# Optimization experiments

Hardware: AMD Instinct MI355X
Metric: run time of the kernel (lower is better)

## Reference

```python
import jax, jax.numpy as jnp
import numpy as np

B, S, H, NH = 2, 2048, 1024, 16
HD = H // NH  # 64


def setup_inputs() -> dict:
    key = jax.random.key(0)
    ks = jax.random.split(key, 9)
    w = lambda k: jax.random.normal(k, (H, H), dtype=jnp.float32) * 0.02  # torch Linear weight [out,in]
    b = lambda k: jax.random.normal(k, (H,), dtype=jnp.float32) * 0.02
    return {
        "hidden_states": jax.random.normal(ks[0], (B, S, H), dtype=jnp.float32),
        "Wq": w(ks[1]), "bq": b(ks[2]),
        "Wk": w(ks[3]), "bk": b(ks[4]),
        "Wv": w(ks[5]), "bv": b(ks[6]),
        "Wo": w(ks[7]), "bo": b(ks[8]),
    }


def reference(hidden_states, Wq, bq, Wk, bk, Wv, bv, Wo, bo):
    b, s, h = hidden_states.shape
    nh, hd = NH, h // NH

    def proj(W, bias):
        y = hidden_states @ W.T + bias  # torch Linear: x W^T + b
        return y.reshape(b, s, nh, hd).transpose(0, 2, 1, 3)  # [b, h, s, d]

    q = proj(Wq, bq)
    k = proj(Wk, bk)
    v = proj(Wv, bv)

    scale = jnp.sqrt(jnp.asarray(hd, dtype=q.dtype))
    scores = jnp.einsum("bhqd,bhkd->bhqk", q, k) / scale  # [b, h, s, s]
    pos = jnp.arange(s)
    causal = pos[:, None] < pos[None, :]  # True where masked (key after query)
    scores = jnp.where(causal[None, None], -jnp.inf, scores)
    attn = jax.nn.softmax(scores, axis=-1)
    out = jnp.einsum("bhqk,bhkd->bhqd", attn, v)
    out = out.transpose(0, 2, 1, 3).reshape(b, s, h)
    return out @ Wo.T + bo
```

## Files before the change

### kernel.cpp

```cpp
#include <hip/hip_runtime.h>
#include <stdint.h>

typedef __bf16 bf16;
typedef __attribute__((ext_vector_type(2))) __bf16 bf16x2;
typedef __attribute__((ext_vector_type(4))) __bf16 bf16x4;
typedef __attribute__((ext_vector_type(8))) __bf16 bf16x8;
typedef __attribute__((ext_vector_type(4))) float f32x4;
typedef __attribute__((ext_vector_type(4))) short s16x4;

#define B_  2
#define S_  2048
#define H_  1024
#define NH_ 16
#define HD_ 64

__device__ __forceinline__ void glds16(const bf16* g, bf16* l) {
  __builtin_amdgcn_global_load_lds(
      (const __attribute__((address_space(1))) uint32_t*)g,
      (__attribute__((address_space(3))) uint32_t*)l, 16, 0, 0);
}

__device__ __forceinline__ f32x4 pv_mfma(bf16x4 a, bf16x4 b, f32x4 c) {
#if __has_builtin(__builtin_amdgcn_mfma_f32_16x16x16bf16_1k)
  union U { bf16x4 h; s16x4 s; };
  U ua; ua.h = a;
  U ub; ub.h = b;
  return __builtin_amdgcn_mfma_f32_16x16x16bf16_1k(ua.s, ub.s, c, 0, 0, 0);
#else
  f32x4 d;
  asm volatile("v_mfma_f32_16x16x16_bf16 %0, %1, %2, %3\n\ts_nop 7\n\ts_nop 7"
               : "=v"(d) : "v"(a), "v"(b), "v"(c));
  return d;
#endif
}

__global__ __launch_bounds__(256) void cvt_f32_bf16(
    const float* __restrict__ s0, bf16* __restrict__ d0, int n0,
    const float* __restrict__ s1, bf16* __restrict__ d1,
    const float* __restrict__ s2, bf16* __restrict__ d2,
    const float* __restrict__ s3, bf16* __restrict__ d3,
    const float* __restrict__ s4, bf16* __restrict__ d4, int nw)
{
  const float* s; bf16* d; int n;
  switch (blockIdx.y) {
    case 0:  s = s0; d = d0; n = n0; break;
    case 1:  s = s1; d = d1; n = nw; break;
    case 2:  s = s2; d = d2; n = nw; break;
    case 3:  s = s3; d = d3; n = nw; break;
    default: s = s4; d = d4; n = nw; break;
  }
  const int i = (blockIdx.x * 256 + threadIdx.x) * 8;
  if (i >= n) return;
  float4 v0 = *(const float4*)(s + i);
  float4 v1 = *(const float4*)(s + i + 4);
  bf16x8 o;
  o[0] = (bf16)v0.x; o[1] = (bf16)v0.y; o[2] = (bf16)v0.z; o[3] = (bf16)v0.w;
  o[4] = (bf16)v1.x; o[5] = (bf16)v1.y; o[6] = (bf16)v1.z; o[7] = (bf16)v1.w;
  *(bf16x8*)(d + i) = o;
}

template <typename TY>
__global__ __launch_bounds__(256) void gemm_bt_bias(
    const bf16* __restrict__ X,
    const bf16* __restrict__ W0, const bf16* __restrict__ W1, const bf16* __restrict__ W2,
    const float* __restrict__ b0, const float* __restrict__ b1, const float* __restrict__ b2,
    TY* __restrict__ Y0, TY* __restrict__ Y1, TY* __restrict__ Y2,
    float ys0, float ys1, float ys2,
    int M, int N, int K)
{
  const bf16* W; const float* bias; TY* Y; float ysc;
  if (blockIdx.z == 0)      { W = W0; bias = b0; Y = Y0; ysc = ys0; }
  else if (blockIdx.z == 1) { W = W1; bias = b1; Y = Y1; ysc = ys1; }
  else                      { W = W2; bias = b2; Y = Y2; ysc = ys2; }

  __shared__ __align__(16) bf16 As[2][128 * 32];
  __shared__ __align__(16) bf16 Bs[2][128 * 32];

  const int tid  = threadIdx.x;
  const int lane = tid & 63;
  const int wave = tid >> 6;
  const int m0 = blockIdx.y * 128;
  const int n0 = blockIdx.x * 128;
  const int wm = (wave >> 1) * 64;
  const int wn = (wave & 1) * 64;

  const int r0 = tid >> 2,            c0 = (tid & 3) * 8;
  const int r1 = (256 + tid) >> 2,    c1 = ((256 + tid) & 3) * 8;
  const int cb0 = (wave * 64) * 8;
  const int cb1 = (256 + wave * 64) * 8;

  f32x4 acc[4][4] = {};

  glds16(X + (size_t)(m0 + r0) * K + c0, &As[0][cb0]);
  glds16(W + (size_t)(n0 + r0) * K + c0, &Bs[0][cb0]);
  glds16(X + (size_t)(m0 + r1) * K + c1, &As[0][cb1]);
  glds16(W + (size_t)(n0 + r1) * K + c1, &Bs[0][cb1]);

  int pb = 0;
  for (int k0 = 0; k0 < K; k0 += 32, pb ^= 1) {
    __syncthreads();

    if (k0 + 32 < K) {
      const int kn = k0 + 32;
      glds16(X + (size_t)(m0 + r0) * K + kn + c0, &As[pb ^ 1][cb0]);
      glds16(W + (size_t)(n0 + r0) * K + kn + c0, &Bs[pb ^ 1][cb0]);
      glds16(X + (size_t)(m0 + r1) * K + kn + c1, &As[pb ^ 1][cb1]);
      glds16(W + (size_t)(n0 + r1) * K + kn + c1, &Bs[pb ^ 1][cb1]);
    }

    bf16x8 a[4], b[4];
#pragma unroll
    for (int i = 0; i < 4; ++i)
      a[i] = *(const bf16x8*)&As[pb][(wm + i * 16 + (lane & 15)) * 32 + (lane >> 4) * 8];
#pragma unroll
    for (int i = 0; i < 4; ++i)
      b[i] = *(const bf16x8*)&Bs[pb][(wn + i * 16 + (lane & 15)) * 32 + (lane >> 4) * 8];
#pragma unroll
    for (int mi = 0; mi < 4; ++mi)
#pragma unroll
      for (int ni = 0; ni < 4; ++ni)
        acc[mi][ni] = __builtin_amdgcn_mfma_f32_16x16x32_bf16(a[mi], b[ni], acc[mi][ni], 0, 0, 0);
  }

#pragma unroll
  for (int mi = 0; mi < 4; ++mi) {
    const int row = m0 + wm + mi * 16 + (lane >> 4) * 4;
#pragma unroll
    for (int ni = 0; ni < 4; ++ni) {
      const int col = n0 + wn + ni * 16 + (lane & 15);
      const float bv = bias[col];
#pragma unroll
      for (int r = 0; r < 4; ++r)
        Y[(size_t)(row + r) * N + col] = (TY)((acc[mi][ni][r] + bv) * ysc);
    }
  }
}


__device__ __forceinline__ void attn_tile_step(
    const bf16* Ksb, const bf16* Vtb, const bf16x8 bq[2], int qrow, int k0,
    bool maskit, float& mr, float& lr, f32x4 oacc[4], int l15, int quad)
{
  f32x4 sacc[8] = {};
  __builtin_amdgcn_s_setprio(1);
#pragma unroll
  for (int ks = 0; ks < 2; ++ks) {
#pragma unroll
    for (int mb = 0; mb < 8; ++mb) {
      const int row = mb * 16 + l15;
      const int ch  = (ks * 4 + quad) ^ (l15 & 7);
      bf16x8 ak = *(const bf16x8*)&Ksb[row * 64 + ch * 8];
      sacc[mb] = __builtin_amdgcn_mfma_f32_16x16x32_bf16(ak, bq[ks], sacc[mb], 0, 0, 0);
    }
  }
  __builtin_amdgcn_s_setprio(0);

  if (maskit) {
#pragma unroll
    for (int mb = 0; mb < 8; ++mb) {
      const int kb = k0 + mb * 16 + quad * 4;
#pragma unroll
      for (int r = 0; r < 4; ++r)
        if (kb + r > qrow) sacc[mb][r] = -1e30f;
    }
  }

  float mx = -1e30f;
#pragma unroll
  for (int mb = 0; mb < 8; ++mb)
    mx = fmaxf(mx, fmaxf(fmaxf(sacc[mb][0], sacc[mb][1]),
                         fmaxf(sacc[mb][2], sacc[mb][3])));
  mx = fmaxf(mx, __shfl_xor(mx, 16, 64));
  mx = fmaxf(mx, __shfl_xor(mx, 32, 64));

  float sum = 0.0f;
  bf16x4 pwv[8];
#pragma unroll
  for (int mb = 0; mb < 8; ++mb) {
    bf16x4 pw;
#pragma unroll
    for (int r = 0; r < 4; ++r) {
      const float p = __builtin_amdgcn_exp2f(sacc[mb][r] - mr);
      sum += p;
      pw[r] = (bf16)p;
    }
    pwv[mb] = pw;
  }
  sum += __shfl_xor(sum, 16, 64);
  sum += __shfl_xor(sum, 32, 64);

  __builtin_amdgcn_s_setprio(1);
#pragma unroll
  for (int mb = 0; mb < 8; ++mb) {
#pragma unroll
    for (int db = 0; db < 4; ++db) {
      const int vch = ((mb * 4 + quad) ^ (l15 & 7)) * 4;
      bf16x4 av = *(const bf16x4*)&Vtb[(db * 16 + l15) * 128 + vch];
      oacc[db] = pv_mfma(av, pwv[mb], oacc[db]);
    }
  }
  __builtin_amdgcn_s_setprio(0);

  lr += sum;
  if (!__all(mx <= mr + 8.0f)) {
    const float mnew  = fmaxf(mr, mx);
    const float alpha = __builtin_amdgcn_exp2f(mr - mnew);
    lr *= alpha;
#pragma unroll
    for (int db = 0; db < 4; ++db)
#pragma unroll
      for (int r = 0; r < 4; ++r) oacc[db][r] *= alpha;
    mr = mnew;
  }
}

__global__ __launch_bounds__(256, 2) void attn_causal(
    const bf16* __restrict__ Q, const bf16* __restrict__ K,
    const bf16* __restrict__ V, bf16* __restrict__ O)
{
  const int lin  = blockIdx.x;
  const int slot = lin >> 3;
  const int bh   = (lin & 7) * 4 + (slot >> 4);
  const int pair = slot & 15;
  const int b    = bh >> 4;
  const int h    = bh & 15;

  const int tid  = threadIdx.x;
  const int lane = tid & 63;
  const int wave = tid >> 6;
  const int quad = lane >> 4;
  const int l15  = lane & 15;
  const size_t headoff = (size_t)b * S_ * H_ + (size_t)h * HD_;
  const bf16* Kp = K + headoff;
  const bf16* Vp = V + headoff;

  __shared__ __align__(16) bf16 Ks[2][128 * 64];
  __shared__ __align__(16) bf16 Vt[2][64 * 128];

  const int qlo = pair, qhi = 31 - pair;
  const int nl  = (qlo >> 1) + 1;
  const int nh  = (qhi >> 1) + 1;
  const int qrowL = qlo * 64 + wave * 16 + l15;
  const int qrowH = qhi * 64 + wave * 16 + l15;

  bf16x8 bqL[2], bqH[2];
  bqL[0] = *(const bf16x8*)(Q + headoff + (size_t)qrowL * H_ + quad * 8);
  bqL[1] = *(const bf16x8*)(Q + headoff + (size_t)qrowL * H_ + 32 + quad * 8);
  bqH[0] = *(const bf16x8*)(Q + headoff + (size_t)qrowH * H_ + quad * 8);
  bqH[1] = *(const bf16x8*)(Q + headoff + (size_t)qrowH * H_ + 32 + quad * 8);

  const int vr = lane * 2;
  const int vc = wave * 16;

#define STAGE_K(k0_, buf_)                                                  \
  {                                                                         \
    _Pragma("unroll")                                                       \
    for (int i = 0; i < 4; ++i) {                                           \
      const int n = i * 256 + tid;                                          \
      const int row = n >> 3;                                               \
      const int cg  = (n & 7) ^ (row & 7);                                  \
      glds16(Kp + (size_t)((k0_) + row) * H_ + cg * 8,                      \
             &Ks[buf_][(i * 256 + wave * 64) * 8]);                         \
    }                                                                       \
  }

#define LOAD_V(k0_)                                                         \
  {                                                                         \
    vreg[0] = *(const bf16x8*)(Vp + (size_t)((k0_) + vr) * H_ + vc);        \
    vreg[1] = *(const bf16x8*)(Vp + (size_t)((k0_) + vr) * H_ + vc + 8);    \
    vreg[2] = *(const bf16x8*)(Vp + (size_t)((k0_) + vr + 1) * H_ + vc);    \
    vreg[3] = *(const bf16x8*)(Vp + (size_t)((k0_) + vr + 1) * H_ + vc + 8);\
  }

#define WRITE_V(buf_)                                                       \
  {                                                                         \
    _Pragma("unroll")                                                       \
    for (int e = 0; e < 8; ++e) {                                           \
      const int sw = (((vr >> 2) ^ e) * 4) + (vr & 3);                      \
      bf16x2 p0; p0[0] = vreg[0][e]; p0[1] = vreg[2][e];                    \
      *(bf16x2*)&Vt[buf_][(vc + e) * 128 + sw] = p0;                        \
      bf16x2 p1; p1[0] = vreg[1][e]; p1[1] = vreg[3][e];                    \
      *(bf16x2*)&Vt[buf_][(vc + 8 + e) * 128 + sw] = p1;                    \
    }                                                                       \
  }

  bf16x8 vreg[4];

  STAGE_K(0, 0);
  LOAD_V(0);
  WRITE_V(0);
  __syncthreads();

  float mrL = 0.0f, lrL = 0.0f, mrH = 0.0f, lrH = 0.0f;
  f32x4 oL[4] = {}, oH[4] = {};

  for (int it = 0; it < nh; ++it) {
    const int c = it & 1;
    const bool pre = (it + 1 < nh);

    if (pre) {
      STAGE_K((it + 1) * 128, c ^ 1);
      LOAD_V((it + 1) * 128);
    }

    attn_tile_step(Ks[c], Vt[c], bqH, qrowH, it * 128, it == nh - 1,
                   mrH, lrH, oH, l15, quad);
    if (it < nl)
      attn_tile_step(Ks[c], Vt[c], bqL, qrowL, it * 128, it == nl - 1,
                     mrL, lrL, oL, l15, quad);

    if (pre) {
      WRITE_V(c ^ 1);
      __syncthreads();
    }
  }

  const float invL = 1.0f / lrL;
#pragma unroll
  for (int db = 0; db < 4; ++db) {
    bf16x4 o;
#pragma unroll
    for (int r = 0; r < 4; ++r) o[r] = (bf16)(oL[db][r] * invL);
    *(bf16x4*)(O + headoff + (size_t)qrowL * H_ + db * 16 + quad * 4) = o;
  }
  const float invH = 1.0f / lrH;
#pragma unroll
  for (int db = 0; db < 4; ++db) {
    bf16x4 o;
#pragma unroll
    for (int r = 0; r < 4; ++r) o[r] = (bf16)(oH[db][r] * invH);
    *(bf16x4*)(O + headoff + (size_t)qrowH * H_ + db * 16 + quad * 4) = o;
  }
#undef STAGE_K
#undef LOAD_V
#undef WRITE_V
}

extern "C" void kernel_launch(void* const* d_in, const int* in_sizes, int n_in,
                              void* d_out, int out_size, void* d_ws, size_t ws_size,
                              hipStream_t stream) {
  const float* hs = (const float*)d_in[0];
  const float* Wq = (const float*)d_in[1]; const float* bq = (const float*)d_in[2];
  const float* Wk = (const float*)d_in[3]; const float* bk = (const float*)d_in[4];
  const float* Wv = (const float*)d_in[5]; const float* bv = (const float*)d_in[6];
  const float* Wo = (const float*)d_in[7]; const float* bo = (const float*)d_in[8];
  float* out = (float*)d_out;

  const size_t elems = (size_t)B_ * S_ * H_;
  const size_t wel   = (size_t)H_ * H_;
  bf16* hsb = (bf16*)d_ws;
  bf16* AO  = hsb;
  bf16* Wqb = hsb + elems;
  bf16* Wkb = Wqb + wel;
  bf16* Wvb = Wkb + wel;
  bf16* Wob = Wvb + wel;
  bf16* Qw  = Wob + wel;
  bf16* Kw  = Qw + elems;
  bf16* Vw  = Kw + elems;

  cvt_f32_bf16<<<dim3(2048, 5), dim3(256), 0, stream>>>(
      hs, hsb, (int)elems, Wq, Wqb, Wk, Wkb, Wv, Wvb, Wo, Wob, (int)wel);

  const int M = B_ * S_;
  const float QSCL = 0.125f * 1.44269504f;
  gemm_bt_bias<bf16><<<dim3(H_ / 128, M / 128, 3), dim3(256), 0, stream>>>(
      hsb, Wqb, Wkb, Wvb, bq, bk, bv, Qw, Kw, Vw, QSCL, 1.0f, 1.0f, M, H_, H_);

  attn_causal<<<dim3(512), dim3(256), 0, stream>>>(Qw, Kw, Vw, AO);

  gemm_bt_bias<float><<<dim3(H_ / 128, M / 128, 1), dim3(256), 0, stream>>>(
      AO, Wob, Wob, Wob, bo, bo, bo, out, out, out, 1.0f, 1.0f, 1.0f, M, H_, H_);
}
```

Measured before the change: 201.1 us.

## Fuse QKV projection into one 256x256-tile GEMM writing an interleaved QKV buffer

Replaces the three-way batched 128x128 QKV GEMM with a single 512-thread kernel. It treats Wq/Wk/Wv as one concatenated 3072x1024 weight (relying on their contiguous workspace layout) and computes 256x256 tiles with a K-step of 64 and phased MFMA/load interleaving. Output goes to a [M,3072] interleaved buffer, and the attention kernel now reads Q, K and V at row stride 3072. The aim is more operand reuse per tile, fewer launches-worth of tiles and better L2 locality via block swizzling. The cost is a larger LDS footprint, higher register use and many barriers per K-step.

```diff
diff --git a/kernel.cpp b/kernel.cpp
--- a/kernel.cpp
+++ b/kernel.cpp
@@ -13,6 +13,7 @@
 #define H_  1024
 #define NH_ 16
 #define HD_ 64
+#define RS  3072
 
 __device__ __forceinline__ void glds16(const bf16* g, bf16* l) {
   __builtin_amdgcn_global_load_lds(
@@ -59,6 +60,150 @@
   *(bf16x8*)(d + i) = o;
 }
 
+__global__ __launch_bounds__(512, 2) void gemm_qkv_8ph(
+    const bf16* __restrict__ X,
+    const bf16* __restrict__ Wc,
+    const float* __restrict__ bq, const float* __restrict__ bk,
+    const float* __restrict__ bv,
+    bf16* __restrict__ Y,
+    float qscl)
+{
+  constexpr int K  = 1024;
+  constexpr int NT = K / 64;
+
+  __shared__ __align__(16) bf16 As[2][256 * 64];
+  __shared__ __align__(16) bf16 Bs[2][256 * 64];
+
+  const int f   = blockIdx.x;
+  const int swz = (f & 7) * 24 + (f >> 3);
+  const int by  = swz / 12, bx = swz % 12;
+  const int m0  = by * 256, n0 = bx * 256;
+
+  const int tid  = threadIdx.x;
+  const int lane = tid & 63;
+  const int wave = tid >> 6;
+  const int quad = lane >> 4;
+  const int l15  = lane & 15;
+  const int wm   = (wave >> 2) * 128;
+  const int wn   = (wave & 3) * 64;
+
+  const int r0  = tid >> 3;
+  const int kc0 = tid & 7;
+
+  const bf16* Xb = X  + (size_t)m0 * K;
+  const bf16* Wb = Wc + (size_t)n0 * K;
+
+  f32x4 acc[8][4] = {};
+
+#define SBAR() asm volatile("s_barrier" ::: "memory")
+#define VM0()  asm volatile("s_waitcnt vmcnt(0)" ::: "memory")
+#define STG(MAT, G, cb_, h)                                                 \
+  { _Pragma("unroll") for (int s = 0; s < 2; ++s) {                         \
+      const int row = (h) * 128 + s * 64 + r0;                              \
+      const int sc  = kc0 ^ (row & 7);                                      \
+      glds16((G) + (size_t)row * K + sc * 8,                                \
+             &MAT[cb_][((h) * 1024 + s * 512 + wave * 64) * 8]); } }
+#define RA(mi, ks) (*(const bf16x8*)&As[cb][(wm + (mi) * 16 + l15) * 64 +   \
+                     ((((ks) * 4 + quad)) ^ (l15 & 7)) * 8])
+#define RB(ni, ks) (*(const bf16x8*)&Bs[cb][(wn + (ni) * 16 + l15) * 64 +   \
+                     ((((ks) * 4 + quad)) ^ (l15 & 7)) * 8])
+#define MFMA(d, x, y) d = __builtin_amdgcn_mfma_f32_16x16x32_bf16(x, y, d, 0, 0, 0)
+
+  STG(As, Xb, 0, 0); STG(As, Xb, 0, 1);
+  STG(Bs, Wb, 0, 0); STG(Bs, Wb, 0, 1);
+  VM0();
+  SBAR();
+
+  for (int t = 0; t < NT; ++t) {
+    const int cb = t & 1, sb = cb ^ 1;
+    const bf16* Xn = Xb + (t + 1) * 64;
+    const bf16* Wn = Wb + (t + 1) * 64;
+    const bool pre = (t + 1 < NT);
+
+    bf16x8 a[4][2], b[4][2];
+
+#pragma unroll
+    for (int mi = 0; mi < 4; ++mi) { a[mi][0] = RA(mi, 0); a[mi][1] = RA(mi, 1); }
+#pragma unroll
+    for (int ni = 0; ni < 2; ++ni) { b[ni][0] = RB(ni, 0); b[ni][1] = RB(ni, 1); }
+    if (pre) { STG(As, Xn, sb, 0); STG(As, Xn, sb, 1); }
+    SBAR();
+    __builtin_amdgcn_s_setprio(1);
+#pragma unroll
+    for (int mi = 0; mi < 4; ++mi)
+#pragma unroll
+      for (int ni = 0; ni < 2; ++ni) {
+        MFMA(acc[mi][ni], a[mi][0], b[ni][0]);
+        MFMA(acc[mi][ni], a[mi][1], b[ni][1]);
+      }
+    __builtin_amdgcn_s_setprio(0);
+    SBAR();
+
+#pragma unroll
+    for (int ni = 2; ni < 4; ++ni) { b[ni][0] = RB(ni, 0); b[ni][1] = RB(ni, 1); }
+    if (pre) { STG(Bs, Wn, sb, 0); STG(Bs, Wn, sb, 1); }
+    SBAR();
+    __builtin_amdgcn_s_setprio(1);
+#pragma unroll
+    for (int mi = 0; mi < 4; ++mi)
+#pragma unroll
+      for (int ni = 2; ni < 4; ++ni) {
+        MFMA(acc[mi][ni], a[mi][0], b[ni][0]);
+        MFMA(acc[mi][ni], a[mi][1], b[ni][1]);
+      }
+    __builtin_amdgcn_s_setprio(0);
+    SBAR();
+
+#pragma unroll
+    for (int mi = 0; mi < 4; ++mi) { a[mi][0] = RA(mi + 4, 0); a[mi][1] = RA(mi + 4, 1); }
+    SBAR();
+    __builtin_amdgcn_s_setprio(1);
+#pragma unroll
+    for (int mi = 0; mi < 4; ++mi)
+#pragma unroll
+      for (int ni = 0; ni < 2; ++ni) {
+        MFMA(acc[mi + 4][ni], a[mi][0], b[ni][0]);
+        MFMA(acc[mi + 4][ni], a[mi][1], b[ni][1]);
+      }
+    __builtin_amdgcn_s_setprio(0);
+    SBAR();
+
+    __builtin_amdgcn_s_setprio(1);
+#pragma unroll
+    for (int mi = 0; mi < 4; ++mi)
+#pragma unroll
+      for (int ni = 2; ni < 4; ++ni) {
+        MFMA(acc[mi + 4][ni], a[mi][0], b[ni][0]);
+        MFMA(acc[mi + 4][ni], a[mi][1], b[ni][1]);
+      }
+    __builtin_amdgcn_s_setprio(0);
+    VM0();
+    SBAR();
+  }
+
+  const int seg = bx >> 2;
+  const float* bias = seg == 0 ? bq : (seg == 1 ? bk : bv);
+  const float ysc = seg == 0 ? qscl : 1.0f;
+#pragma unroll
+  for (int mi = 0; mi < 8; ++mi) {
+    const int row = m0 + wm + mi * 16 + quad * 4;
+#pragma unroll
+    for (int ni = 0; ni < 4; ++ni) {
+      const int col = n0 + wn + ni * 16 + l15;
+      const float bvv = bias[col & 1023];
+#pragma unroll
+      for (int r = 0; r < 4; ++r)
+        Y[(size_t)(row + r) * RS + col] = (bf16)((acc[mi][ni][r] + bvv) * ysc);
+    }
+  }
+#undef SBAR
+#undef VM0
+#undef STG
+#undef RA
+#undef RB
+#undef MFMA
+}
+
 template <typename TY>
 __global__ __launch_bounds__(256) void gemm_bt_bias(
     const bf16* __restrict__ X,
@@ -136,7 +281,6 @@
   }
 }
 
-
 __device__ __forceinline__ void attn_tile_step(
     const bf16* Ksb, const bf16* Vtb, const bf16x8 bq[2], int qrow, int k0,
     bool maskit, float& mr, float& lr, f32x4 oacc[4], int l15, int quad)
@@ -215,8 +359,8 @@
 }
 
 __global__ __launch_bounds__(256, 2) void attn_causal(
-    const bf16* __restrict__ Q, const bf16* __restrict__ K,
-    const bf16* __restrict__ V, bf16* __restrict__ O)
+    const bf16* __restrict__ QKV,
+    bf16* __restrict__ O)
 {
   const int lin  = blockIdx.x;
   const int slot = lin >> 3;
@@ -230,9 +374,11 @@
   const int wave = tid >> 6;
   const int quad = lane >> 4;
   const int l15  = lane & 15;
-  const size_t headoff = (size_t)b * S_ * H_ + (size_t)h * HD_;
-  const bf16* Kp = K + headoff;
-  const bf16* Vp = V + headoff;
+  const size_t headq = (size_t)b * S_ * RS + (size_t)h * HD_;
+  const size_t heado = (size_t)b * S_ * H_ + (size_t)h * HD_;
+  const bf16* Qp = QKV + headq;
+  const bf16* Kp = QKV + headq + 1024;
+  const bf16* Vp = QKV + headq + 2048;
 
   __shared__ __align__(16) bf16 Ks[2][128 * 64];
   __shared__ __align__(16) bf16 Vt[2][64 * 128];
@@ -244,10 +390,10 @@
   const int qrowH = qhi * 64 + wave * 16 + l15;
 
   bf16x8 bqL[2], bqH[2];
-  bqL[0] = *(const bf16x8*)(Q + headoff + (size_t)qrowL * H_ + quad * 8);
-  bqL[1] = *(const bf16x8*)(Q + headoff + (size_t)qrowL * H_ + 32 + quad * 8);
-  bqH[0] = *(const bf16x8*)(Q + headoff + (size_t)qrowH * H_ + quad * 8);
-  bqH[1] = *(const bf16x8*)(Q + headoff + (size_t)qrowH * H_ + 32 + quad * 8);
+  bqL[0] = *(const bf16x8*)(Qp + (size_t)qrowL * RS + quad * 8);
+  bqL[1] = *(const bf16x8*)(Qp + (size_t)qrowL * RS + 32 + quad * 8);
+  bqH[0] = *(const bf16x8*)(Qp + (size_t)qrowH * RS + quad * 8);
+  bqH[1] = *(const bf16x8*)(Qp + (size_t)qrowH * RS + 32 + quad * 8);
 
   const int vr = lane * 2;
   const int vc = wave * 16;
@@ -259,17 +405,17 @@
       const int n = i * 256 + tid;                                          \
       const int row = n >> 3;                                               \
       const int cg  = (n & 7) ^ (row & 7);                                  \
-      glds16(Kp + (size_t)((k0_) + row) * H_ + cg * 8,                      \
+      glds16(Kp + (size_t)((k0_) + row) * RS + cg * 8,                      \
              &Ks[buf_][(i * 256 + wave * 64) * 8]);                         \
     }                                                                       \
   }
 
 #define LOAD_V(k0_)                                                         \
   {                                                                         \
-    vreg[0] = *(const bf16x8*)(Vp + (size_t)((k0_) + vr) * H_ + vc);        \
-    vreg[1] = *(const bf16x8*)(Vp + (size_t)((k0_) + vr) * H_ + vc + 8);    \
-    vreg[2] = *(const bf16x8*)(Vp + (size_t)((k0_) + vr + 1) * H_ + vc);    \
-    vreg[3] = *(const bf16x8*)(Vp + (size_t)((k0_) + vr + 1) * H_ + vc + 8);\
+    vreg[0] = *(const bf16x8*)(Vp + (size_t)((k0_) + vr) * RS + vc);        \
+    vreg[1] = *(const bf16x8*)(Vp + (size_t)((k0_) + vr) * RS + vc + 8);    \
+    vreg[2] = *(const bf16x8*)(Vp + (size_t)((k0_) + vr + 1) * RS + vc);    \
+    vreg[3] = *(const bf16x8*)(Vp + (size_t)((k0_) + vr + 1) * RS + vc + 8);\
   }
 
 #define WRITE_V(buf_)                                                       \
@@ -321,7 +467,7 @@
     bf16x4 o;
 #pragma unroll
     for (int r = 0; r < 4; ++r) o[r] = (bf16)(oL[db][r] * invL);
-    *(bf16x4*)(O + headoff + (size_t)qrowL * H_ + db * 16 + quad * 4) = o;
+    *(bf16x4*)(O + heado + (size_t)qrowL * H_ + db * 16 + quad * 4) = o;
   }
   const float invH = 1.0f / lrH;
 #pragma unroll
@@ -329,7 +475,7 @@
     bf16x4 o;
 #pragma unroll
     for (int r = 0; r < 4; ++r) o[r] = (bf16)(oH[db][r] * invH);
-    *(bf16x4*)(O + headoff + (size_t)qrowH * H_ + db * 16 + quad * 4) = o;
+    *(bf16x4*)(O + heado + (size_t)qrowH * H_ + db * 16 + quad * 4) = o;
   }
 #undef STAGE_K
 #undef LOAD_V
@@ -348,25 +494,24 @@
 
   const size_t elems = (size_t)B_ * S_ * H_;
   const size_t wel   = (size_t)H_ * H_;
-  bf16* hsb = (bf16*)d_ws;
-  bf16* AO  = hsb;
-  bf16* Wqb = hsb + elems;
-  bf16* Wkb = Wqb + wel;
-  bf16* Wvb = Wkb + wel;
-  bf16* Wob = Wvb + wel;
-  bf16* Qw  = Wob + wel;
-  bf16* Kw  = Qw + elems;
-  bf16* Vw  = Kw + elems;
+  bf16* hsb  = (bf16*)d_ws;
+  bf16* AO   = hsb;
+  bf16* Wqb  = hsb + elems;
+  bf16* Wkb  = Wqb + wel;
+  bf16* Wvb  = Wkb + wel;
+  bf16* Wob  = Wvb + wel;
+  bf16* Ycat = Wob + wel;
 
   cvt_f32_bf16<<<dim3(2048, 5), dim3(256), 0, stream>>>(
       hs, hsb, (int)elems, Wq, Wqb, Wk, Wkb, Wv, Wvb, Wo, Wob, (int)wel);
 
   const int M = B_ * S_;
   const float QSCL = 0.125f * 1.44269504f;
-  gemm_bt_bias<bf16><<<dim3(H_ / 128, M / 128, 3), dim3(256), 0, stream>>>(
-      hsb, Wqb, Wkb, Wvb, bq, bk, bv, Qw, Kw, Vw, QSCL, 1.0f, 1.0f, M, H_, H_);
-
-  attn_causal<<<dim3(512), dim3(256), 0, stream>>>(Qw, Kw, Vw, AO);
+
+  gemm_qkv_8ph<<<dim3(192), dim3(512), 0, stream>>>(
+      hsb, Wqb, bq, bk, bv, Ycat, QSCL);
+
+  attn_causal<<<dim3(512), dim3(256), 0, stream>>>(Ycat, AO);
 
   gemm_bt_bias<float><<<dim3(H_ / 128, M / 128, 1), dim3(256), 0, stream>>>(
       AO, Wob, Wob, Wob, bo, bo, bo, out, out, out, 1.0f, 1.0f, 1.0f, M, H_, H_);
```

Measured after the change: 200.7 us. No clear change (-0.2%).

## Replace projection GEMMs with 256x256-tile eight-phase pipelined MFMA kernels

Applied to the files above, without the earlier changes.

Both the fused QKV projection and the output projection move to a new GEMM with 256x256 block tiles, 512 threads and 64-wide K chunks. LDS rows are XOR-swizzled, and each K step is split into phases that interleave LDS reads, async global-to-LDS prefetch and MFMA bursts, separated by raw barriers and priority hints. QKV now treats the contiguous Wq/Wk/Wv buffers as one 3072-column weight and picks the output tensor and bias per column segment. A block-index swizzle improves L2 locality. The larger tiles increase operand reuse and cut global traffic, but they launch far fewer blocks (192 and 64) than the device has CUs and use about 128KB of LDS per block, so occupancy and CU fill may suffer.

```diff
diff --git a/kernel.cpp b/kernel.cpp
--- a/kernel.cpp
+++ b/kernel.cpp
@@ -59,83 +59,177 @@
   *(bf16x8*)(d + i) = o;
 }
 
-template <typename TY>
-__global__ __launch_bounds__(256) void gemm_bt_bias(
-    const bf16* __restrict__ X,
-    const bf16* __restrict__ W0, const bf16* __restrict__ W1, const bf16* __restrict__ W2,
-    const float* __restrict__ b0, const float* __restrict__ b1, const float* __restrict__ b2,
-    TY* __restrict__ Y0, TY* __restrict__ Y1, TY* __restrict__ Y2,
-    float ys0, float ys1, float ys2,
-    int M, int N, int K)
+#define G8_SBAR() asm volatile("s_barrier" ::: "memory")
+#define G8_VM0()  asm volatile("s_waitcnt vmcnt(0)" ::: "memory")
+#define G8_STG(MAT, G, cb_, h)                                              \
+  { _Pragma("unroll") for (int s = 0; s < 2; ++s) {                         \
+      const int row = (h) * 128 + s * 64 + r0;                              \
+      const int sc  = kc0 ^ (row & 7);                                      \
+      glds16((G) + (size_t)row * 1024 + sc * 8,                             \
+             &MAT[cb_][((h) * 1024 + s * 512 + wave * 64) * 8]); } }
+#define G8_RA(mi, ks) (*(const bf16x8*)&As[cb][(wm + (mi) * 16 + l15) * 64 + \
+                     ((((ks) * 4 + quad)) ^ (l15 & 7)) * 8])
+#define G8_RB(ni, ks) (*(const bf16x8*)&Bs[cb][(wn + (ni) * 16 + l15) * 64 + \
+                     ((((ks) * 4 + quad)) ^ (l15 & 7)) * 8])
+#define G8_MFMA(d, x, y) d = __builtin_amdgcn_mfma_f32_16x16x32_bf16(x, y, d, 0, 0, 0)
+
+#define G8_BODY()                                                           \
+  f32x4 acc[8][4] = {};                                                     \
+  G8_STG(As, Xb, 0, 0); G8_STG(As, Xb, 0, 1);                               \
+  G8_STG(Bs, Wb, 0, 0); G8_STG(Bs, Wb, 0, 1);                               \
+  G8_VM0();                                                                 \
+  G8_SBAR();                                                                \
+  for (int t = 0; t < 16; ++t) {                                            \
+    const int cb = t & 1, sb = cb ^ 1;                                      \
+    const bf16* Xn = Xb + (t + 1) * 64;                                     \
+    const bf16* Wn = Wb + (t + 1) * 64;                                     \
+    const bool pre = (t + 1 < 16);                                          \
+    bf16x8 a[4][2], b[4][2];                                                \
+    _Pragma("unroll")                                                       \
+    for (int mi = 0; mi < 4; ++mi) { a[mi][0] = G8_RA(mi, 0); a[mi][1] = G8_RA(mi, 1); } \
+    _Pragma("unroll")                                                       \
+    for (int ni = 0; ni < 2; ++ni) { b[ni][0] = G8_RB(ni, 0); b[ni][1] = G8_RB(ni, 1); } \
+    if (pre) { G8_STG(As, Xn, sb, 0); G8_STG(As, Xn, sb, 1); }              \
+    G8_SBAR();                                                              \
+    __builtin_amdgcn_s_setprio(1);                                          \
+    _Pragma("unroll")                                                       \
+    for (int mi = 0; mi < 4; ++mi)                                          \
+      _Pragma("unroll")                                                     \
+      for (int ni = 0; ni < 2; ++ni) {                                      \
+        G8_MFMA(acc[mi][ni], a[mi][0], b[ni][0]);                           \
+        G8_MFMA(acc[mi][ni], a[mi][1], b[ni][1]);                           \
+      }                                                                     \
+    __builtin_amdgcn_s_setprio(0);                                          \
+    G8_SBAR();                                                              \
+    _Pragma("unroll")                                                       \
+    for (int ni = 2; ni < 4; ++ni) { b[ni][0] = G8_RB(ni, 0); b[ni][1] = G8_RB(ni, 1); } \
+    if (pre) { G8_STG(Bs, Wn, sb, 0); G8_STG(Bs, Wn, sb, 1); }              \
+    G8_SBAR();                                                              \
+    __builtin_amdgcn_s_setprio(1);                                          \
+    _Pragma("unroll")                                                       \
+    for (int mi = 0; mi < 4; ++mi)                                          \
+      _Pragma("unroll")                                                     \
+      for (int ni = 2; ni < 4; ++ni) {                                      \
+        G8_MFMA(acc[mi][ni], a[mi][0], b[ni][0]);                           \
+        G8_MFMA(acc[mi][ni], a[mi][1], b[ni][1]);                           \
+      }                                                                     \
+    __builtin_amdgcn_s_setprio(0);                                          \
+    G8_SBAR();                                                              \
+    _Pragma("unroll")                                                       \
+    for (int mi = 0; mi < 4; ++mi) { a[mi][0] = G8_RA(mi + 4, 0); a[mi][1] = G8_RA(mi + 4, 1); } \
+    G8_SBAR();                                                              \
+    __builtin_amdgcn_s_setprio(1);                                          \
+    _Pragma("unroll")                                                       \
+    for (int mi = 0; mi < 4; ++mi)                                          \
+      _Pragma("unroll")                                                     \
+      for (int ni = 0; ni < 2; ++ni) {                                      \
+        G8_MFMA(acc[mi + 4][ni], a[mi][0], b[ni][0]);                       \
+        G8_MFMA(acc[mi + 4][ni], a[mi][1], b[ni][1]);                       \
+      }                                                                     \
+    __builtin_amdgcn_s_setprio(0);                                          \
+    G8_SBAR();                                                              \
+    __builtin_amdgcn_s_setprio(1);                                          \
+    _Pragma("unroll")                                                       \
+    for (int mi = 0; mi < 4; ++mi)                                          \
+      _Pragma("unroll")                                                     \
+      for (int ni = 2; ni < 4; ++ni) {                                      \
+        G8_MFMA(acc[mi + 4][ni], a[mi][0], b[ni][0]);                       \
+        G8_MFMA(acc[mi + 4][ni], a[mi][1], b[ni][1]);                       \
+      }                                                                     \
+    __builtin_amdgcn_s_setprio(0);                                          \
+    G8_VM0();                                                               \
+    G8_SBAR();                                                              \
+  }
+
+__global__ __launch_bounds__(512, 2) void gemm_qkv_8ph(
+    const bf16* __restrict__ X, const bf16* __restrict__ Wc,
+    const float* __restrict__ bq, const float* __restrict__ bk,
+    const float* __restrict__ bv,
+    bf16* __restrict__ Yq, bf16* __restrict__ Yk, bf16* __restrict__ Yv,
+    float qscl)
 {
-  const bf16* W; const float* bias; TY* Y; float ysc;
-  if (blockIdx.z == 0)      { W = W0; bias = b0; Y = Y0; ysc = ys0; }
-  else if (blockIdx.z == 1) { W = W1; bias = b1; Y = Y1; ysc = ys1; }
-  else                      { W = W2; bias = b2; Y = Y2; ysc = ys2; }
-
-  __shared__ __align__(16) bf16 As[2][128 * 32];
-  __shared__ __align__(16) bf16 Bs[2][128 * 32];
+  __shared__ __align__(16) bf16 As[2][256 * 64];
+  __shared__ __align__(16) bf16 Bs[2][256 * 64];
+
+  const int f   = blockIdx.x;
+  const int swz = (f & 7) * 24 + (f >> 3);
+  const int by  = swz / 12, bx = swz % 12;
+  const int m0  = by * 256, n0 = bx * 256;
 
   const int tid  = threadIdx.x;
   const int lane = tid & 63;
   const int wave = tid >> 6;
-  const int m0 = blockIdx.y * 128;
-  const int n0 = blockIdx.x * 128;
-  const int wm = (wave >> 1) * 64;
-  const int wn = (wave & 1) * 64;
-
-  const int r0 = tid >> 2,            c0 = (tid & 3) * 8;
-  const int r1 = (256 + tid) >> 2,    c1 = ((256 + tid) & 3) * 8;
-  const int cb0 = (wave * 64) * 8;
-  const int cb1 = (256 + wave * 64) * 8;
-
-  f32x4 acc[4][4] = {};
-
-  glds16(X + (size_t)(m0 + r0) * K + c0, &As[0][cb0]);
-  glds16(W + (size_t)(n0 + r0) * K + c0, &Bs[0][cb0]);
-  glds16(X + (size_t)(m0 + r1) * K + c1, &As[0][cb1]);
-  glds16(W + (size_t)(n0 + r1) * K + c1, &Bs[0][cb1]);
-
-  int pb = 0;
-  for (int k0 = 0; k0 < K; k0 += 32, pb ^= 1) {
-    __syncthreads();
-
-    if (k0 + 32 < K) {
-      const int kn = k0 + 32;
-      glds16(X + (size_t)(m0 + r0) * K + kn + c0, &As[pb ^ 1][cb0]);
-      glds16(W + (size_t)(n0 + r0) * K + kn + c0, &Bs[pb ^ 1][cb0]);
-      glds16(X + (size_t)(m0 + r1) * K + kn + c1, &As[pb ^ 1][cb1]);
-      glds16(W + (size_t)(n0 + r1) * K + kn + c1, &Bs[pb ^ 1][cb1]);
-    }
-
-    bf16x8 a[4], b[4];
-#pragma unroll
-    for (int i = 0; i < 4; ++i)
-      a[i] = *(const bf16x8*)&As[pb][(wm + i * 16 + (lane & 15)) * 32 + (lane >> 4) * 8];
-#pragma unroll
-    for (int i = 0; i < 4; ++i)
-      b[i] = *(const bf16x8*)&Bs[pb][(wn + i * 16 + (lane & 15)) * 32 + (lane >> 4) * 8];
-#pragma unroll
-    for (int mi = 0; mi < 4; ++mi)
-#pragma unroll
-      for (int ni = 0; ni < 4; ++ni)
-        acc[mi][ni] = __builtin_amdgcn_mfma_f32_16x16x32_bf16(a[mi], b[ni], acc[mi][ni], 0, 0, 0);
-  }
-
-#pragma unroll
-  for (int mi = 0; mi < 4; ++mi) {
-    const int row = m0 + wm + mi * 16 + (lane >> 4) * 4;
+  const int quad = lane >> 4;
+  const int l15  = lane & 15;
+  const int wm   = (wave >> 2) * 128;
+  const int wn   = (wave & 3) * 64;
+  const int r0   = tid >> 3;
+  const int kc0  = tid & 7;
+
+  const bf16* Xb = X  + (size_t)m0 * 1024;
+  const bf16* Wb = Wc + (size_t)n0 * 1024;
+
+  G8_BODY();
+
+  const int seg = bx >> 2;
+  const float* bias = seg == 0 ? bq : (seg == 1 ? bk : bv);
+  bf16* Yp = seg == 0 ? Yq : (seg == 1 ? Yk : Yv);
+  const float ysc = seg == 0 ? qscl : 1.0f;
+  const int nc0 = n0 - seg * 1024;
+#pragma unroll
+  for (int mi = 0; mi < 8; ++mi) {
+    const int row = m0 + wm + mi * 16 + quad * 4;
 #pragma unroll
     for (int ni = 0; ni < 4; ++ni) {
-      const int col = n0 + wn + ni * 16 + (lane & 15);
-      const float bv = bias[col];
+      const int col = nc0 + wn + ni * 16 + l15;
+      const float bvv = bias[col];
 #pragma unroll
       for (int r = 0; r < 4; ++r)
-        Y[(size_t)(row + r) * N + col] = (TY)((acc[mi][ni][r] + bv) * ysc);
-    }
-  }
-}
-
+        Yp[(size_t)(row + r) * H_ + col] = (bf16)((acc[mi][ni][r] + bvv) * ysc);
+    }
+  }
+}
+
+__global__ __launch_bounds__(512, 2) void gemm_o_8ph(
+    const bf16* __restrict__ X, const bf16* __restrict__ W,
+    const float* __restrict__ bias, float* __restrict__ Y)
+{
+  __shared__ __align__(16) bf16 As[2][256 * 64];
+  __shared__ __align__(16) bf16 Bs[2][256 * 64];
+
+  const int f   = blockIdx.x;
+  const int swz = (f & 7) * 8 + (f >> 3);
+  const int by  = swz >> 2, bx = swz & 3;
+  const int m0  = by * 256, n0 = bx * 256;
+
+  const int tid  = threadIdx.x;
+  const int lane = tid & 63;
+  const int wave = tid >> 6;
+  const int quad = lane >> 4;
+  const int l15  = lane & 15;
+  const int wm   = (wave >> 2) * 128;
+  const int wn   = (wave & 3) * 64;
+  const int r0   = tid >> 3;
+  const int kc0  = tid & 7;
+
+  const bf16* Xb = X + (size_t)m0 * 1024;
+  const bf16* Wb = W + (size_t)n0 * 1024;
+
+  G8_BODY();
+
+#pragma unroll
+  for (int mi = 0; mi < 8; ++mi) {
+    const int row = m0 + wm + mi * 16 + quad * 4;
+#pragma unroll
+    for (int ni = 0; ni < 4; ++ni) {
+      const int col = n0 + wn + ni * 16 + l15;
+      const float bvv = bias[col];
+#pragma unroll
+      for (int r = 0; r < 4; ++r)
+        Y[(size_t)(row + r) * H_ + col] = acc[mi][ni][r] + bvv;
+    }
+  }
+}
 
 __device__ __forceinline__ void attn_tile_step(
     const bf16* Ksb, const bf16* Vtb, const bf16x8 bq[2], int qrow, int k0,
@@ -361,13 +455,12 @@
   cvt_f32_bf16<<<dim3(2048, 5), dim3(256), 0, stream>>>(
       hs, hsb, (int)elems, Wq, Wqb, Wk, Wkb, Wv, Wvb, Wo, Wob, (int)wel);
 
-  const int M = B_ * S_;
   const float QSCL = 0.125f * 1.44269504f;
-  gemm_bt_bias<bf16><<<dim3(H_ / 128, M / 128, 3), dim3(256), 0, stream>>>(
-      hsb, Wqb, Wkb, Wvb, bq, bk, bv, Qw, Kw, Vw, QSCL, 1.0f, 1.0f, M, H_, H_);
+
+  gemm_qkv_8ph<<<dim3(192), dim3(512), 0, stream>>>(
+      hsb, Wqb, bq, bk, bv, Qw, Kw, Vw, QSCL);
 
   attn_causal<<<dim3(512), dim3(256), 0, stream>>>(Qw, Kw, Vw, AO);
 
-  gemm_bt_bias<float><<<dim3(H_ / 128, M / 128, 1), dim3(256), 0, stream>>>(
-      AO, Wob, Wob, Wob, bo, bo, bo, out, out, out, 1.0f, 1.0f, 1.0f, M, H_, H_);
-}
+  gemm_o_8ph<<<dim3(64), dim3(512), 0, stream>>>(AO, Wob, bo, out);
+}
```

Result: slower. 209.1 us (+4.0%).

## Fuse fp32-to-bf16 conversion into QKV and output projection GEMM tile loads

Applied to the files above, without the earlier changes.

Removes the separate conversion kernel that wrote bf16 copies of the hidden states and all four weight matrices. The QKV GEMM now loads fp32 tiles into registers, converts them and stores bf16 into shared memory while computing on the previous buffer. The output GEMM does the same for Wo and keeps the async global-to-LDS path for the bf16 attention output. This saves a kernel launch and a full fp32 read plus bf16 write and re-read, at the cost of more register pressure, twice the global bytes per GEMM tile load, and redundant conversion across blocks.

```diff
diff --git a/kernel.cpp b/kernel.cpp
--- a/kernel.cpp
+++ b/kernel.cpp
@@ -34,45 +34,103 @@
 #endif
 }
 
-__global__ __launch_bounds__(256) void cvt_f32_bf16(
-    const float* __restrict__ s0, bf16* __restrict__ d0, int n0,
-    const float* __restrict__ s1, bf16* __restrict__ d1,
-    const float* __restrict__ s2, bf16* __restrict__ d2,
-    const float* __restrict__ s3, bf16* __restrict__ d3,
-    const float* __restrict__ s4, bf16* __restrict__ d4, int nw)
+__device__ __forceinline__ void cvt16_store(const float4 v[4], bf16* dst) {
+  bf16x8 o0, o1;
+  o0[0] = (bf16)v[0].x; o0[1] = (bf16)v[0].y; o0[2] = (bf16)v[0].z; o0[3] = (bf16)v[0].w;
+  o0[4] = (bf16)v[1].x; o0[5] = (bf16)v[1].y; o0[6] = (bf16)v[1].z; o0[7] = (bf16)v[1].w;
+  o1[0] = (bf16)v[2].x; o1[1] = (bf16)v[2].y; o1[2] = (bf16)v[2].z; o1[3] = (bf16)v[2].w;
+  o1[4] = (bf16)v[3].x; o1[5] = (bf16)v[3].y; o1[6] = (bf16)v[3].z; o1[7] = (bf16)v[3].w;
+  *(bf16x8*)(dst)     = o0;
+  *(bf16x8*)(dst + 8) = o1;
+}
+
+#define LD4(dst, src)                                                       \
+  { dst[0] = *(const float4*)(src);      dst[1] = *(const float4*)((src) + 4); \
+    dst[2] = *(const float4*)((src) + 8); dst[3] = *(const float4*)((src) + 12); }
+
+__global__ __launch_bounds__(256) void gemm_qkv_f32(
+    const float* __restrict__ X,
+    const float* __restrict__ Wqf, const float* __restrict__ Wkf,
+    const float* __restrict__ Wvf,
+    const float* __restrict__ bq, const float* __restrict__ bk,
+    const float* __restrict__ bv,
+    bf16* __restrict__ Yq, bf16* __restrict__ Yk, bf16* __restrict__ Yv,
+    float qscl)
 {
-  const float* s; bf16* d; int n;
-  switch (blockIdx.y) {
-    case 0:  s = s0; d = d0; n = n0; break;
-    case 1:  s = s1; d = d1; n = nw; break;
-    case 2:  s = s2; d = d2; n = nw; break;
-    case 3:  s = s3; d = d3; n = nw; break;
-    default: s = s4; d = d4; n = nw; break;
-  }
-  const int i = (blockIdx.x * 256 + threadIdx.x) * 8;
-  if (i >= n) return;
-  float4 v0 = *(const float4*)(s + i);
-  float4 v1 = *(const float4*)(s + i + 4);
-  bf16x8 o;
-  o[0] = (bf16)v0.x; o[1] = (bf16)v0.y; o[2] = (bf16)v0.z; o[3] = (bf16)v0.w;
-  o[4] = (bf16)v1.x; o[5] = (bf16)v1.y; o[6] = (bf16)v1.z; o[7] = (bf16)v1.w;
-  *(bf16x8*)(d + i) = o;
-}
-
-template <typename TY>
-__global__ __launch_bounds__(256) void gemm_bt_bias(
-    const bf16* __restrict__ X,
-    const bf16* __restrict__ W0, const bf16* __restrict__ W1, const bf16* __restrict__ W2,
-    const float* __restrict__ b0, const float* __restrict__ b1, const float* __restrict__ b2,
-    TY* __restrict__ Y0, TY* __restrict__ Y1, TY* __restrict__ Y2,
-    float ys0, float ys1, float ys2,
-    int M, int N, int K)
+  __shared__ __align__(16) bf16 As[2][128 * 32];
+  __shared__ __align__(16) bf16 Bs[2][128 * 32];
+
+  const int tid  = threadIdx.x;
+  const int lane = tid & 63;
+  const int wave = tid >> 6;
+
+  const int m0  = blockIdx.y * 128;
+  const int n0g = blockIdx.x * 128;
+  const int seg = n0g >> 10;
+  const float* W    = seg == 0 ? Wqf : (seg == 1 ? Wkf : Wvf);
+  const float* bias = seg == 0 ? bq  : (seg == 1 ? bk  : bv);
+  bf16*        Y    = seg == 0 ? Yq  : (seg == 1 ? Yk  : Yv);
+  const float  ysc  = seg == 0 ? qscl : 1.0f;
+  const int    n0   = n0g & 1023;
+
+  const int wm = (wave >> 1) * 64;
+  const int wn = (wave & 1) * 64;
+
+  const int sr = tid >> 1, sc = (tid & 1) * 16;
+  const float* Xs = X + (size_t)(m0 + sr) * 1024 + sc;
+  const float* Ws = W + (size_t)(n0 + sr) * 1024 + sc;
+  const int sdst = sr * 32 + sc;
+
+  f32x4 acc[4][4] = {};
+  float4 va[4], vb[4];
+
+  LD4(va, Xs); LD4(vb, Ws);
+  cvt16_store(va, &As[0][sdst]);
+  cvt16_store(vb, &Bs[0][sdst]);
+
+  int pb = 0;
+  for (int k0 = 0; k0 < 1024; k0 += 32, pb ^= 1) {
+    __syncthreads();
+    const bool pre = k0 + 32 < 1024;
+    if (pre) { LD4(va, Xs + k0 + 32); LD4(vb, Ws + k0 + 32); }
+
+    bf16x8 a[4], b[4];
+#pragma unroll
+    for (int i = 0; i < 4; ++i)
+      a[i] = *(const bf16x8*)&As[pb][(wm + i * 16 + (lane & 15)) * 32 + (lane >> 4) * 8];
+#pragma unroll
+    for (int i = 0; i < 4; ++i)
+      b[i] = *(const bf16x8*)&Bs[pb][(wn + i * 16 + (lane & 15)) * 32 + (lane >> 4) * 8];
+#pragma unroll
+    for (int mi = 0; mi < 4; ++mi)
+#pragma unroll
+      for (int ni = 0; ni < 4; ++ni)
+        acc[mi][ni] = __builtin_amdgcn_mfma_f32_16x16x32_bf16(a[mi], b[ni], acc[mi][ni], 0, 0, 0);
+
+    if (pre) {
+      cvt16_store(va, &As[pb ^ 1][sdst]);
+      cvt16_store(vb, &Bs[pb ^ 1][sdst]);
+    }
+  }
+
+#pragma unroll
+  for (int mi = 0; mi < 4; ++mi) {
+    const int row = m0 + wm + mi * 16 + (lane >> 4) * 4;
+#pragma unroll
+    for (int ni = 0; ni < 4; ++ni) {
+      const int col = n0 + wn + ni * 16 + (lane & 15);
+      const float bvv = bias[col];
+#pragma unroll
+      for (int r = 0; r < 4; ++r)
+        Y[(size_t)(row + r) * 1024 + col] = (bf16)((acc[mi][ni][r] + bvv) * ysc);
+    }
+  }
+}
+
+__global__ __launch_bounds__(256) void gemm_o_f32w(
+    const bf16* __restrict__ X, const float* __restrict__ W,
+    const float* __restrict__ bias, float* __restrict__ Y)
 {
-  const bf16* W; const float* bias; TY* Y; float ysc;
-  if (blockIdx.z == 0)      { W = W0; bias = b0; Y = Y0; ysc = ys0; }
-  else if (blockIdx.z == 1) { W = W1; bias = b1; Y = Y1; ysc = ys1; }
-  else                      { W = W2; bias = b2; Y = Y2; ysc = ys2; }
-
   __shared__ __align__(16) bf16 As[2][128 * 32];
   __shared__ __align__(16) bf16 Bs[2][128 * 32];
 
@@ -89,23 +147,27 @@
   const int cb0 = (wave * 64) * 8;
   const int cb1 = (256 + wave * 64) * 8;
 
+  const int sr = tid >> 1, sc = (tid & 1) * 16;
+  const float* Ws = W + (size_t)(n0 + sr) * 1024 + sc;
+  const int sdst = sr * 32 + sc;
+
   f32x4 acc[4][4] = {};
-
-  glds16(X + (size_t)(m0 + r0) * K + c0, &As[0][cb0]);
-  glds16(W + (size_t)(n0 + r0) * K + c0, &Bs[0][cb0]);
-  glds16(X + (size_t)(m0 + r1) * K + c1, &As[0][cb1]);
-  glds16(W + (size_t)(n0 + r1) * K + c1, &Bs[0][cb1]);
+  float4 vb[4];
+
+  glds16(X + (size_t)(m0 + r0) * 1024 + c0, &As[0][cb0]);
+  glds16(X + (size_t)(m0 + r1) * 1024 + c1, &As[0][cb1]);
+  LD4(vb, Ws);
+  cvt16_store(vb, &Bs[0][sdst]);
 
   int pb = 0;
-  for (int k0 = 0; k0 < K; k0 += 32, pb ^= 1) {
+  for (int k0 = 0; k0 < 1024; k0 += 32, pb ^= 1) {
     __syncthreads();
-
-    if (k0 + 32 < K) {
+    const bool pre = k0 + 32 < 1024;
+    if (pre) {
       const int kn = k0 + 32;
-      glds16(X + (size_t)(m0 + r0) * K + kn + c0, &As[pb ^ 1][cb0]);
-      glds16(W + (size_t)(n0 + r0) * K + kn + c0, &Bs[pb ^ 1][cb0]);
-      glds16(X + (size_t)(m0 + r1) * K + kn + c1, &As[pb ^ 1][cb1]);
-      glds16(W + (size_t)(n0 + r1) * K + kn + c1, &Bs[pb ^ 1][cb1]);
+      glds16(X + (size_t)(m0 + r0) * 1024 + kn + c0, &As[pb ^ 1][cb0]);
+      glds16(X + (size_t)(m0 + r1) * 1024 + kn + c1, &As[pb ^ 1][cb1]);
+      LD4(vb, Ws + kn);
     }
 
     bf16x8 a[4], b[4];
@@ -120,6 +182,8 @@
 #pragma unroll
       for (int ni = 0; ni < 4; ++ni)
         acc[mi][ni] = __builtin_amdgcn_mfma_f32_16x16x32_bf16(a[mi], b[ni], acc[mi][ni], 0, 0, 0);
+
+    if (pre) cvt16_store(vb, &Bs[pb ^ 1][sdst]);
   }
 
 #pragma unroll
@@ -128,14 +192,13 @@
 #pragma unroll
     for (int ni = 0; ni < 4; ++ni) {
       const int col = n0 + wn + ni * 16 + (lane & 15);
-      const float bv = bias[col];
+      const float bvv = bias[col];
 #pragma unroll
       for (int r = 0; r < 4; ++r)
-        Y[(size_t)(row + r) * N + col] = (TY)((acc[mi][ni][r] + bv) * ysc);
-    }
-  }
-}
-
+        Y[(size_t)(row + r) * 1024 + col] = acc[mi][ni][r] + bvv;
+    }
+  }
+}
 
 __device__ __forceinline__ void attn_tile_step(
     const bf16* Ksb, const bf16* Vtb, const bf16x8 bq[2], int qrow, int k0,
@@ -347,27 +410,17 @@
   float* out = (float*)d_out;
 
   const size_t elems = (size_t)B_ * S_ * H_;
-  const size_t wel   = (size_t)H_ * H_;
-  bf16* hsb = (bf16*)d_ws;
-  bf16* AO  = hsb;
-  bf16* Wqb = hsb + elems;
-  bf16* Wkb = Wqb + wel;
-  bf16* Wvb = Wkb + wel;
-  bf16* Wob = Wvb + wel;
-  bf16* Qw  = Wob + wel;
-  bf16* Kw  = Qw + elems;
-  bf16* Vw  = Kw + elems;
-
-  cvt_f32_bf16<<<dim3(2048, 5), dim3(256), 0, stream>>>(
-      hs, hsb, (int)elems, Wq, Wqb, Wk, Wkb, Wv, Wvb, Wo, Wob, (int)wel);
-
-  const int M = B_ * S_;
+  bf16* Qw = (bf16*)d_ws;
+  bf16* Kw = Qw + elems;
+  bf16* Vw = Kw + elems;
+  bf16* AO = Vw + elems;
+
   const float QSCL = 0.125f * 1.44269504f;
-  gemm_bt_bias<bf16><<<dim3(H_ / 128, M / 128, 3), dim3(256), 0, stream>>>(
-      hsb, Wqb, Wkb, Wvb, bq, bk, bv, Qw, Kw, Vw, QSCL, 1.0f, 1.0f, M, H_, H_);
+
+  gemm_qkv_f32<<<dim3(24, 32), dim3(256), 0, stream>>>(
+      hs, Wq, Wk, Wv, bq, bk, bv, Qw, Kw, Vw, QSCL);
 
   attn_causal<<<dim3(512), dim3(256), 0, stream>>>(Qw, Kw, Vw, AO);
 
-  gemm_bt_bias<float><<<dim3(H_ / 128, M / 128, 1), dim3(256), 0, stream>>>(
-      AO, Wob, Wob, Wob, bo, bo, bo, out, out, out, 1.0f, 1.0f, 1.0f, M, H_, H_);
-}
+  gemm_o_f32w<<<dim3(8, 32), dim3(256), 0, stream>>>(AO, Wo, bo, out);
+}
```

New measurement: 247.5 us. 1.23x slower.
